# Kernel tuning notes

Measured on AMD Instinct MI355X. Metric: run time of the kernel, lower is better.

The kernel has to match this reference:

```python
import jax, jax.numpy as jnp
import numpy as np

_SAMPLING_EPS = 1e-05
_FP16_TINY = float(np.finfo(np.float16).tiny)  # masked_fill value used by the torch code


def _token_mask(tokens, num_seqs, vocab_size):
    # bin-count via scatter-add into width vocab+1 (padding id == vocab), then mask
    rows = jnp.arange(num_seqs)[:, None]
    counts = jnp.zeros((num_seqs, vocab_size + 1), jnp.int32).at[rows, tokens].add(1)
    return counts[:, :vocab_size] > 0


def setup_inputs() -> dict:
    key = jax.random.key(0)
    ks = jax.random.split(key, 9)
    B, V, PL, OL = 128, 128000, 2048, 256
    logits = jax.random.normal(ks[0], (B, V), dtype=jnp.float32) * 4.0
    prompt_tokens = jax.random.randint(ks[1], (B, PL), 0, V, dtype=jnp.int64)
    output_tokens = jax.random.randint(ks[2], (B, OL), 0, V, dtype=jnp.int64)
    presence_penalties = jax.random.uniform(ks[3], (B,), dtype=jnp.float32)
    frequency_penalties = jax.random.uniform(ks[4], (B,), dtype=jnp.float32)
    repetition_penalties = 1.0 + 0.3 * jax.random.uniform(ks[5], (B,), dtype=jnp.float32)
    temperature = 0.1 + 0.9 * jax.random.uniform(ks[6], (B,), dtype=jnp.float32)
    top_k = jax.random.randint(ks[7], (B,), 1, 100, dtype=jnp.int64)
    top_p = 0.5 + 0.49 * jax.random.uniform(ks[8], (B,), dtype=jnp.float32)
    return {
        "logits": logits,
        "prompt_tokens": prompt_tokens,
        "output_tokens": output_tokens,
        "presence_penalties": presence_penalties,
        "frequency_penalties": frequency_penalties,
        "repetition_penalties": repetition_penalties,
        "temperature": temperature,
        "top_k": top_k,
        "top_p": top_p,
    }


def reference(logits, prompt_tokens, output_tokens, presence_penalties,
              frequency_penalties, repetition_penalties, temperature,
              top_k, top_p):
    B, V = logits.shape
    logits = logits.astype(jnp.float32)

    # --- penalties (NOTE: torch code computes frequency counts but never applies
    # frequency_penalties; we faithfully do the same) ---
    prompt_mask = _token_mask(prompt_tokens, B, V)
    output_mask = _token_mask(output_tokens, B, V)
    pen = jnp.where(prompt_mask | output_mask, repetition_penalties[:, None], 1.0)
    logits = jnp.where(logits > 0, logits / pen, logits * pen)
    logits = logits - presence_penalties[:, None] * output_mask.astype(jnp.float32)

    # --- temperature ---
    temp = jnp.where(temperature < _SAMPLING_EPS, 1.0, temperature)
    logits = logits / temp[:, None]

    # --- top-k / top-p via ascending sort (mirrors torch implementation) ---
    idx = jnp.argsort(logits, axis=-1)                      # ascending
    ls = jnp.take_along_axis(logits, idx, axis=-1)
    thr_pos = (V - top_k.astype(jnp.int32))[:, None]
    thr = jnp.take_along_axis(ls, thr_pos, axis=-1)         # [B,1]
    ls = jnp.where(ls < thr, _FP16_TINY, ls)
    probs_sort = jax.nn.softmax(ls, axis=-1)
    csum = jnp.cumsum(probs_sort, axis=-1)
    tp_mask = csum <= (1.0 - top_p)[:, None]
    tp_mask = tp_mask.at[:, -1].set(False)
    ls = jnp.where(tp_mask, _FP16_TINY, ls)

    # unsort back to original vocab order
    rows = jnp.arange(B)[:, None]
    out_logits = jnp.zeros_like(logits).at[rows, idx].set(ls)

    probs = jax.nn.softmax(out_logits, axis=-1)
    return probs, prompt_mask, output_mask
```

## Files before the change

### kernel.cpp

```cpp
#include <hip/hip_runtime.h>
#include <math.h>

#define B   128
#define V   128000
#define WPR 4000
#define PL  2048
#define OL  256
#define BPR 25
#define ITERS 5
#define TLOC 128
#define GMAX 240
#define CAP  6144
#define FP16_TINY 6.103515625e-05f
#define QZ   1.80f

#define HBINS 4096
#define HIDX(b) ((b) + ((b) >> 4))
#define HSZ (HBINS + (HBINS >> 4))

__device__ __forceinline__ unsigned key_of(float f) {
    unsigned u = __float_as_uint(f);
    unsigned m = (unsigned)(((int)u) >> 31) | 0x80000000u;
    return u ^ m;
}
__device__ __forceinline__ float key_inv(unsigned k) {
    unsigned u = (k & 0x80000000u) ? (k ^ 0x80000000u) : ~k;
    return __uint_as_float(u);
}

__device__ __forceinline__ float xform(float x, int pm, int om,
                                       float rp, float rrp, float pres, float itt) {
#pragma clang fp contract(off)
    float m = (pm | om) ? ((x > 0.0f) ? rrp : rp) : 1.0f;
    float l = x * m;
    if (om) l = l - pres;
    return l * itt;
}

__device__ __forceinline__ unsigned wave_suffix_u(unsigned x, int lane) {
#pragma unroll
    for (int o = 1; o < 64; o <<= 1) {
        unsigned a = __shfl_down(x, o);
        if (lane + o < 64) x += a;
    }
    return x;
}
__device__ __forceinline__ unsigned wave_prefix_u(unsigned x, int lane) {
#pragma unroll
    for (int o = 1; o < 64; o <<= 1) {
        unsigned a = __shfl_up(x, o);
        if (lane >= o) x += a;
    }
    return x;
}
__device__ __forceinline__ double wave_suffix_d(double x, int lane) {
#pragma unroll
    for (int o = 1; o < 64; o <<= 1) {
        double a = __shfl_down(x, o);
        if (lane + o < 64) x += a;
    }
    return x;
}
__device__ __forceinline__ double wave_sum_d(double x) {
#pragma unroll
    for (int o = 1; o < 64; o <<= 1) x += __shfl_xor(x, o);
    return x;
}
__device__ __forceinline__ unsigned wave_sum_u(unsigned x) {
#pragma unroll
    for (int o = 1; o < 64; o <<= 1) x += __shfl_xor(x, o);
    return x;
}

__global__ __launch_bounds__(256) void k_scatter(const int* __restrict__ ptok,
                                                 const int* __restrict__ otok,
                                                 unsigned* __restrict__ bitP,
                                                 unsigned* __restrict__ bitO,
                                                 unsigned* __restrict__ cnt) {
    __shared__ unsigned mp[WPR];
    __shared__ unsigned mo[WPR];
    int r = blockIdx.x;
    int t = threadIdx.x;
    for (int i = t; i < WPR; i += 256) { mp[i] = 0u; mo[i] = 0u; }
    if (t == 0) cnt[r] = 0u;
    __syncthreads();
    const int* prow = ptok + (size_t)r * PL;
    const int* orow = otok + (size_t)r * OL;
    for (int i = t; i < PL; i += 256) {
        int tok = prow[i];
        if ((unsigned)tok < (unsigned)V) atomicOr(&mp[tok >> 5], 1u << (tok & 31));
    }
    for (int i = t; i < OL; i += 256) {
        int tok = orow[i];
        if ((unsigned)tok < (unsigned)V) atomicOr(&mo[tok >> 5], 1u << (tok & 31));
    }
    __syncthreads();
    unsigned* bpo = bitP + (size_t)r * WPR;
    unsigned* boo = bitO + (size_t)r * WPR;
    for (int i = t; i < WPR; i += 256) { bpo[i] = mp[i]; boo[i] = mo[i]; }
}

__global__ __launch_bounds__(256) void k_main(
    const float* __restrict__ logits,
    const unsigned* __restrict__ bitP, const unsigned* __restrict__ bitO,
    const float* __restrict__ rep, const float* __restrict__ pres,
    const float* __restrict__ temp,
    float* __restrict__ outPm, float* __restrict__ outOm,
    unsigned* __restrict__ cnt, unsigned long long* __restrict__ cand)
{
    __shared__ unsigned h[HSZ];
    __shared__ unsigned wsum[4];
    __shared__ int s_beta;
    __shared__ unsigned s_base, s_total;
    int r = blockIdx.y;
    int c0 = blockIdx.x * (ITERS * 1024);
    int t = threadIdx.x;
    int lane = t & 63, wid = t >> 6;
    float rp = rep[r], pp = pres[r];
    float tt = temp[r]; tt = (tt < 1e-5f) ? 1.0f : tt;
    float rrp = 1.0f / rp;
    float itt = 1.0f / tt;
    const float* lrow = logits + (size_t)r * V;
    float* pmrow = outPm + (size_t)r * V;
    float* omrow = outOm + (size_t)r * V;
    const unsigned* bp = bitP + (size_t)r * WPR;
    const unsigned* bo = bitO + (size_t)r * WPR;
    uint4 kv4[ITERS];
#pragma unroll
    for (int it = 0; it < ITERS; it++) {
        int i = c0 + it * 1024 + t * 4;
        float4 x = *(const float4*)(lrow + i);
        unsigned wp = bp[i >> 5], wo = bo[i >> 5];
        int sh = i & 31;
        float xs[4] = {x.x, x.y, x.z, x.w};
        unsigned ks[4];
        float fp[4], fo[4];
#pragma unroll
        for (int j = 0; j < 4; j++) {
            int p = (wp >> (sh + j)) & 1;
            int o = (wo >> (sh + j)) & 1;
            float l = xform(xs[j], p, o, rp, rrp, pp, itt);
            ks[j] = key_of(l);
            fp[j] = (float)p; fo[j] = (float)o;
        }
        kv4[it] = make_uint4(ks[0], ks[1], ks[2], ks[3]);
        *(float4*)(pmrow + i) = make_float4(fp[0], fp[1], fp[2], fp[3]);
        *(float4*)(omrow + i) = make_float4(fo[0], fo[1], fo[2], fo[3]);
    }
    unsigned gk = key_of(QZ * 4.0f * itt);
    unsigned myc = 0;
#pragma unroll
    for (int it = 0; it < ITERS; it++) {
        unsigned ks[4] = {kv4[it].x, kv4[it].y, kv4[it].z, kv4[it].w};
#pragma unroll
        for (int j = 0; j < 4; j++)
            if (ks[j] >= gk) myc++;
    }
    unsigned pfx = wave_prefix_u(myc, lane);
    if (lane == 63) wsum[wid] = pfx;
    __syncthreads();
    unsigned pv = pfx;
#pragma unroll
    for (int w2 = 0; w2 < 4; w2++) if (w2 < wid) pv += wsum[w2];
    if (t == 255) s_total = pv;
    __syncthreads();
    unsigned total = s_total;
    unsigned betaKey;
    if (total >= TLOC && total <= GMAX) {
        betaKey = gk;
    } else {
        for (int i = t; i < HSZ; i += 256) h[i] = 0u;
        __syncthreads();
#pragma unroll
        for (int it = 0; it < ITERS; it++) {
            unsigned ks[4] = {kv4[it].x, kv4[it].y, kv4[it].z, kv4[it].w};
#pragma unroll
            for (int j = 0; j < 4; j++)
                atomicAdd(&h[HIDX(ks[j] >> 20)], 1u);
        }
        __syncthreads();
        unsigned cs = 0;
#pragma unroll
        for (int j = 0; j < 16; j++) cs += h[HIDX(t * 16 + j)];
        unsigned sfx = wave_suffix_u(cs, lane);
        if (lane == 0) wsum[wid] = sfx;
        __syncthreads();
        unsigned suf = sfx;
#pragma unroll
        for (int w2 = 0; w2 < 4; w2++) if (w2 > wid) suf += wsum[w2];
        unsigned Snext = suf - cs;
        if (suf >= TLOC && Snext < TLOC) {
            unsigned run = Snext;
            int beta = t * 16;
            for (int j = 15; j >= 0; j--) {
                run += h[HIDX(t * 16 + j)];
                if (run >= TLOC) { beta = t * 16 + j; break; }
            }
            s_beta = beta;
        }
        __syncthreads();
        betaKey = ((unsigned)s_beta) << 20;
        myc = 0;
#pragma unroll
        for (int it = 0; it < ITERS; it++) {
            unsigned ks[4] = {kv4[it].x, kv4[it].y, kv4[it].z, kv4[it].w};
#pragma unroll
            for (int j = 0; j < 4; j++)
                if (ks[j] >= betaKey) myc++;
        }
        __syncthreads();
        pfx = wave_prefix_u(myc, lane);
        if (lane == 63) wsum[wid] = pfx;
        __syncthreads();
        pv = pfx;
#pragma unroll
        for (int w2 = 0; w2 < 4; w2++) if (w2 < wid) pv += wsum[w2];
    }
    if (t == 255) s_base = atomicAdd(&cnt[r], pv);
    __syncthreads();
    unsigned w = s_base + (pv - myc);
#pragma unroll
    for (int it = 0; it < ITERS; it++) {
        unsigned ks[4] = {kv4[it].x, kv4[it].y, kv4[it].z, kv4[it].w};
#pragma unroll
        for (int j = 0; j < 4; j++) {
            unsigned key = ks[j];
            if (key >= betaKey) {
                if (w < (unsigned)CAP) {
                    int idx = c0 + it * 1024 + t * 4 + j;
                    cand[(size_t)r * CAP + w] =
                        ((unsigned long long)key << 32) | (unsigned)idx;
                }
                w++;
            }
        }
    }
}

__global__ __launch_bounds__(256) void k_select(
    const unsigned* __restrict__ cnt, const unsigned long long* __restrict__ cand,
    const int* __restrict__ topk, const float* __restrict__ topp,
    float4* __restrict__ params, int* __restrict__ idxc,
    unsigned* __restrict__ kn, int* __restrict__ kidx, float* __restrict__ kprob)
{
    __shared__ unsigned long long list[CAP];
    __shared__ unsigned long long kv[256];
    __shared__ unsigned rh[256];
    __shared__ double wD[4];
    __shared__ unsigned wU[4];
    __shared__ unsigned s_prefix, s_krem, s_kcnt;
    int r = blockIdx.x;
    int t = threadIdx.x;
    int lane = t & 63, wid = t >> 6;
    int n = (int)min(cnt[r], (unsigned)CAP);
    const unsigned long long* crow = cand + (size_t)r * CAP;
    for (int i = t; i < n; i += 256) list[i] = crow[i];
    int k = topk[r]; k = max(1, min(k, 127));
    if (t == 0) { s_prefix = 0u; s_krem = (unsigned)k; }
    __syncthreads();
    for (int round = 3; round >= 0; round--) {
        int shift = round * 8;
        unsigned prefix = s_prefix;
        unsigned krem = s_krem;
        unsigned maskAbove = (round == 3) ? 0u : (0xFFFFFFFFu << (shift + 8));
        rh[t] = 0u;
        __syncthreads();
        for (int i = t; i < n; i += 256) {
            unsigned key = (unsigned)(list[i] >> 32);
            if ((key & maskAbove) == (prefix & maskAbove))
                atomicAdd(&rh[(key >> shift) & 255u], 1u);
        }
        __syncthreads();
        unsigned vv = rh[t];
        unsigned sfx = wave_suffix_u(vv, lane);
        if (lane == 0) wU[wid] = sfx;
        __syncthreads();
        unsigned suf = sfx;
#pragma unroll
        for (int w2 = 0; w2 < 4; w2++) if (w2 > wid) suf += wU[w2];
        unsigned Sx = suf - vv;
        if (suf >= krem && Sx < krem) {
            s_prefix = prefix | ((unsigned)t << shift);
            s_krem = krem - Sx;
        }
        __syncthreads();
    }
    unsigned thrkey = s_prefix;
    if (t == 0) s_kcnt = 0u;
    __syncthreads();
    for (int i = t; i < n; i += 256) {
        if ((unsigned)(list[i] >> 32) >= thrkey) {
            unsigned pos = atomicAdd(&s_kcnt, 1u);
            if (pos < 256u) kv[pos] = list[i];
        }
    }
    __syncthreads();
    int K = (int)min(s_kcnt, 256u);
    if (t >= K) kv[t] = 0ULL;
    __syncthreads();
    unsigned long long my = kv[t];
    int rank = 0;
#pragma unroll 8
    for (int i = 0; i < 256; i++) rank += (kv[i] > my) ? 1 : 0;
    __syncthreads();
    if (t < K) kv[rank] = my;
    __syncthreads();
    float Mxf = key_inv((unsigned)(kv[0] >> 32));
    double MxD = (double)Mxf;
    double e_t = (t < K) ? exp((double)key_inv((unsigned)(kv[t] >> 32)) - MxD)
                         : 0.0;
    double red = wave_sum_d(e_t);
    if (lane == 0) wD[wid] = red;
    __syncthreads();
    double S = wD[0] + wD[1] + wD[2] + wD[3];
    __syncthreads();
    double sv = wave_suffix_d(e_t, lane);
    if (lane == 0) wD[wid] = sv;
    __syncthreads();
    double suf_t = sv;
#pragma unroll
    for (int w2 = 0; w2 < 4; w2++) if (w2 > wid) suf_t += wD[w2];
    double e_tinyD = exp((double)FP16_TINY - MxD);
    double Z1 = (double)(V - K) * e_tinyD + S;
    double base = (double)(V - K) * e_tinyD / Z1;
    double thresh = 1.0 - (double)topp[r];
    unsigned flag = (t >= 1 && t < K && (base + suf_t / Z1) <= thresh) ? 1u : 0u;
    unsigned fr = wave_sum_u(flag);
    if (lane == 0) wU[wid] = fr;
    __syncthreads();
    int cm = (int)(wU[0] + wU[1] + wU[2] + wU[3]);
    int ns = K - cm;
    __syncthreads();
    double e2 = (t < ns) ? e_t : 0.0;
    double r2 = wave_sum_d(e2);
    if (lane == 0) wD[wid] = r2;
    __syncthreads();
    double S2 = wD[0] + wD[1] + wD[2] + wD[3];
    unsigned bkey = (unsigned)(kv[ns - 1] >> 32);
    float v_b = key_inv(bkey);
    float tiny_e = expf(FP16_TINY - Mxf);
    double Z2 = (double)(V - ns) * (double)tiny_e + S2;
    float invZ2 = (float)(1.0 / Z2);
    if (t == 0) {
        params[r] = make_float4(v_b, Mxf, invZ2, tiny_e * invZ2);
        idxc[r] = (int)(kv[ns - 1] & 0xFFFFFFFFu);
        kn[r] = (unsigned)ns;
    }
    if (t < ns) {
        unsigned long long e = kv[t];
        unsigned key = (unsigned)(e >> 32);
        kidx[(size_t)r * 256 + t] = (int)(e & 0xFFFFFFFFu);
        kprob[(size_t)r * 256 + t] = expf(key_inv(key) - Mxf) * invZ2;
    }
}

__global__ __launch_bounds__(256) void k_final(
    const float4* __restrict__ params, const unsigned* __restrict__ kn,
    const int* __restrict__ kidx, const float* __restrict__ kprob,
    float* __restrict__ probs)
{
    int r = blockIdx.y;
    int c0 = blockIdx.x * (ITERS * 1024);
    int t = threadIdx.x;
    float ptiny = params[r].w;
    float* orow = probs + (size_t)r * V;
    float4 pv4 = make_float4(ptiny, ptiny, ptiny, ptiny);
#pragma unroll
    for (int it = 0; it < ITERS; it++) {
        int i = c0 + it * 1024 + t * 4;
        *(float4*)(orow + i) = pv4;
    }
    __syncthreads();
    int ns = (int)kn[r];
    int hi = c0 + ITERS * 1024;
    for (int i = t; i < ns; i += 256) {
        int idx = kidx[(size_t)r * 256 + i];
        if (idx >= c0 && idx < hi) orow[idx] = kprob[(size_t)r * 256 + i];
    }
}

extern "C" void kernel_launch(void* const* d_in, const int* in_sizes, int n_in,
                              void* d_out, int out_size, void* d_ws, size_t ws_size,
                              hipStream_t stream) {
    const float* logits = (const float*)d_in[0];
    const int* ptok     = (const int*)d_in[1];
    const int* otok     = (const int*)d_in[2];
    const float* pres   = (const float*)d_in[3];
    const float* rep    = (const float*)d_in[5];
    const float* temp   = (const float*)d_in[6];
    const int* topk     = (const int*)d_in[7];
    const float* topp   = (const float*)d_in[8];

    float* out_probs = (float*)d_out;
    float* out_pm = out_probs + (size_t)B * V;
    float* out_om = out_pm + (size_t)B * V;

    unsigned* ws0 = (unsigned*)d_ws;
    float4* params = (float4*)d_ws;
    int* idxc = (int*)(ws0 + 512);
    unsigned* bitP = ws0 + 768;
    unsigned* bitO = bitP + B * WPR;
    unsigned* cnt  = bitO + B * WPR;
    unsigned long long* cand =
        (unsigned long long*)(cnt + B + 64);
    unsigned* kn   = (unsigned*)(cand + (size_t)B * CAP);
    int* kidx      = (int*)(kn + B);
    float* kprob   = (float*)(kidx + B * 256);

    k_scatter<<<B, 256, 0, stream>>>(ptok, otok, bitP, bitO, cnt);

    dim3 g(BPR, B);
    k_main<<<g, 256, 0, stream>>>(logits, bitP, bitO, rep, pres, temp,
                                  out_pm, out_om, cnt, cand);
    k_select<<<B, 256, 0, stream>>>(cnt, cand, topk, topp, params, idxc,
                                    kn, kidx, kprob);
    k_final<<<g, 256, 0, stream>>>(params, kn, kidx, kprob, out_probs);
}
```

Baseline: 296.5 us.

## Fuse top-k/top-p selection into main kernel via last-block-done counter

Removes the separate k_select launch. Each row's last finishing k_main block, found with a per-row atomic done counter and threadfences, now runs the radix select, sort and top-p computation. Candidates are read straight from global memory rather than staged in shared memory. This saves one kernel launch and lets selection for early-finishing rows overlap with other rows' main work, at the cost of extra shared memory in k_main and repeated global reads of the candidate list.

```diff
diff --git a/kernel.cpp b/kernel.cpp
--- a/kernel.cpp
+++ b/kernel.cpp
@@ -76,13 +76,14 @@
                                                  const int* __restrict__ otok,
                                                  unsigned* __restrict__ bitP,
                                                  unsigned* __restrict__ bitO,
-                                                 unsigned* __restrict__ cnt) {
+                                                 unsigned* __restrict__ cnt,
+                                                 unsigned* __restrict__ done) {
     __shared__ unsigned mp[WPR];
     __shared__ unsigned mo[WPR];
     int r = blockIdx.x;
     int t = threadIdx.x;
     for (int i = t; i < WPR; i += 256) { mp[i] = 0u; mo[i] = 0u; }
-    if (t == 0) cnt[r] = 0u;
+    if (t == 0) { cnt[r] = 0u; done[r] = 0u; }
     __syncthreads();
     const int* prow = ptok + (size_t)r * PL;
     const int* orow = otok + (size_t)r * OL;
@@ -105,13 +106,23 @@
     const unsigned* __restrict__ bitP, const unsigned* __restrict__ bitO,
     const float* __restrict__ rep, const float* __restrict__ pres,
     const float* __restrict__ temp,
+    const int* __restrict__ topk, const float* __restrict__ topp,
     float* __restrict__ outPm, float* __restrict__ outOm,
-    unsigned* __restrict__ cnt, unsigned long long* __restrict__ cand)
+    unsigned* __restrict__ cnt, unsigned* __restrict__ done,
+    unsigned long long* __restrict__ cand,
+    float4* __restrict__ params, unsigned* __restrict__ kn,
+    int* __restrict__ kidx, float* __restrict__ kprob)
 {
     __shared__ unsigned h[HSZ];
     __shared__ unsigned wsum[4];
     __shared__ int s_beta;
-    __shared__ unsigned s_base, s_total;
+    __shared__ unsigned s_base, s_total, s_last;
+    __shared__ unsigned long long kvv[256];
+    __shared__ unsigned rh[256];
+    __shared__ double wD[4];
+    __shared__ unsigned wU[4];
+    __shared__ unsigned s_prefix, s_krem, s_kcnt;
+
     int r = blockIdx.y;
     int c0 = blockIdx.x * (ITERS * 1024);
     int t = threadIdx.x;
@@ -235,26 +246,15 @@
             }
         }
     }
-}
-
-__global__ __launch_bounds__(256) void k_select(
-    const unsigned* __restrict__ cnt, const unsigned long long* __restrict__ cand,
-    const int* __restrict__ topk, const float* __restrict__ topp,
-    float4* __restrict__ params, int* __restrict__ idxc,
-    unsigned* __restrict__ kn, int* __restrict__ kidx, float* __restrict__ kprob)
-{
-    __shared__ unsigned long long list[CAP];
-    __shared__ unsigned long long kv[256];
-    __shared__ unsigned rh[256];
-    __shared__ double wD[4];
-    __shared__ unsigned wU[4];
-    __shared__ unsigned s_prefix, s_krem, s_kcnt;
-    int r = blockIdx.x;
-    int t = threadIdx.x;
-    int lane = t & 63, wid = t >> 6;
+    __threadfence();
+    __syncthreads();
+    if (t == 0) s_last = atomicAdd(&done[r], 1u);
+    __syncthreads();
+    if (s_last != BPR - 1) return;
+    __threadfence();
+
     int n = (int)min(cnt[r], (unsigned)CAP);
     const unsigned long long* crow = cand + (size_t)r * CAP;
-    for (int i = t; i < n; i += 256) list[i] = crow[i];
     int k = topk[r]; k = max(1, min(k, 127));
     if (t == 0) { s_prefix = 0u; s_krem = (unsigned)k; }
     __syncthreads();
@@ -266,7 +266,7 @@
         rh[t] = 0u;
         __syncthreads();
         for (int i = t; i < n; i += 256) {
-            unsigned key = (unsigned)(list[i] >> 32);
+            unsigned key = (unsigned)(crow[i] >> 32);
             if ((key & maskAbove) == (prefix & maskAbove))
                 atomicAdd(&rh[(key >> shift) & 255u], 1u);
         }
@@ -289,25 +289,25 @@
     if (t == 0) s_kcnt = 0u;
     __syncthreads();
     for (int i = t; i < n; i += 256) {
-        if ((unsigned)(list[i] >> 32) >= thrkey) {
+        if ((unsigned)(crow[i] >> 32) >= thrkey) {
             unsigned pos = atomicAdd(&s_kcnt, 1u);
-            if (pos < 256u) kv[pos] = list[i];
+            if (pos < 256u) kvv[pos] = crow[i];
         }
     }
     __syncthreads();
     int K = (int)min(s_kcnt, 256u);
-    if (t >= K) kv[t] = 0ULL;
-    __syncthreads();
-    unsigned long long my = kv[t];
+    if (t >= K) kvv[t] = 0ULL;
+    __syncthreads();
+    unsigned long long my = kvv[t];
     int rank = 0;
 #pragma unroll 8
-    for (int i = 0; i < 256; i++) rank += (kv[i] > my) ? 1 : 0;
-    __syncthreads();
-    if (t < K) kv[rank] = my;
-    __syncthreads();
-    float Mxf = key_inv((unsigned)(kv[0] >> 32));
+    for (int i = 0; i < 256; i++) rank += (kvv[i] > my) ? 1 : 0;
+    __syncthreads();
+    if (t < K) kvv[rank] = my;
+    __syncthreads();
+    float Mxf = key_inv((unsigned)(kvv[0] >> 32));
     double MxD = (double)Mxf;
-    double e_t = (t < K) ? exp((double)key_inv((unsigned)(kv[t] >> 32)) - MxD)
+    double e_t = (t < K) ? exp((double)key_inv((unsigned)(kvv[t] >> 32)) - MxD)
                          : 0.0;
     double red = wave_sum_d(e_t);
     if (lane == 0) wD[wid] = red;
@@ -336,18 +336,16 @@
     if (lane == 0) wD[wid] = r2;
     __syncthreads();
     double S2 = wD[0] + wD[1] + wD[2] + wD[3];
-    unsigned bkey = (unsigned)(kv[ns - 1] >> 32);
-    float v_b = key_inv(bkey);
     float tiny_e = expf(FP16_TINY - Mxf);
     double Z2 = (double)(V - ns) * (double)tiny_e + S2;
     float invZ2 = (float)(1.0 / Z2);
     if (t == 0) {
-        params[r] = make_float4(v_b, Mxf, invZ2, tiny_e * invZ2);
-        idxc[r] = (int)(kv[ns - 1] & 0xFFFFFFFFu);
+        params[r] = make_float4(key_inv((unsigned)(kvv[ns - 1] >> 32)), Mxf,
+                                invZ2, tiny_e * invZ2);
         kn[r] = (unsigned)ns;
     }
     if (t < ns) {
-        unsigned long long e = kv[t];
+        unsigned long long e = kvv[t];
         unsigned key = (unsigned)(e >> 32);
         kidx[(size_t)r * 256 + t] = (int)(e & 0xFFFFFFFFu);
         kprob[(size_t)r * 256 + t] = expf(key_inv(key) - Mxf) * invZ2;
@@ -397,7 +395,7 @@
 
     unsigned* ws0 = (unsigned*)d_ws;
     float4* params = (float4*)d_ws;
-    int* idxc = (int*)(ws0 + 512);
+    unsigned* done = ws0 + 512;
     unsigned* bitP = ws0 + 768;
     unsigned* bitO = bitP + B * WPR;
     unsigned* cnt  = bitO + B * WPR;
@@ -407,12 +405,11 @@
     int* kidx      = (int*)(kn + B);
     float* kprob   = (float*)(kidx + B * 256);
 
-    k_scatter<<<B, 256, 0, stream>>>(ptok, otok, bitP, bitO, cnt);
+    k_scatter<<<B, 256, 0, stream>>>(ptok, otok, bitP, bitO, cnt, done);
 
     dim3 g(BPR, B);
     k_main<<<g, 256, 0, stream>>>(logits, bitP, bitO, rep, pres, temp,
-                                  out_pm, out_om, cnt, cand);
-    k_select<<<B, 256, 0, stream>>>(cnt, cand, topk, topp, params, idxc,
-                                    kn, kidx, kprob);
+                                  topk, topp, out_pm, out_om,
+                                  cnt, done, cand, params, kn, kidx, kprob);
     k_final<<<g, 256, 0, stream>>>(params, kn, kidx, kprob, out_probs);
 }
```

Result: slower. 852.0 us (+187.4%).

## Fuse token bitmap construction into main kernel using per-slice shared bitmaps

Applied to the files above, without the earlier changes.

Removes the separate scatter kernel and its global bitmap buffers. Each main-kernel block now scans the row's prompt and output tokens and builds a small shared-memory bitmap covering only its slice. A memset replaces the counter reset. This avoids one launch and the global bitmap write and read, at the cost of every block rereading all tokens of its row and doing redundant range checks.

```diff
diff --git a/kernel.cpp b/kernel.cpp
--- a/kernel.cpp
+++ b/kernel.cpp
@@ -3,11 +3,12 @@
 
 #define B   128
 #define V   128000
-#define WPR 4000
 #define PL  2048
 #define OL  256
 #define BPR 25
 #define ITERS 5
+#define SLICE (ITERS * 1024)
+#define SW  160
 #define TLOC 128
 #define GMAX 240
 #define CAP  6144
@@ -72,50 +73,37 @@
     return x;
 }
 
-__global__ __launch_bounds__(256) void k_scatter(const int* __restrict__ ptok,
-                                                 const int* __restrict__ otok,
-                                                 unsigned* __restrict__ bitP,
-                                                 unsigned* __restrict__ bitO,
-                                                 unsigned* __restrict__ cnt) {
-    __shared__ unsigned mp[WPR];
-    __shared__ unsigned mo[WPR];
-    int r = blockIdx.x;
-    int t = threadIdx.x;
-    for (int i = t; i < WPR; i += 256) { mp[i] = 0u; mo[i] = 0u; }
-    if (t == 0) cnt[r] = 0u;
-    __syncthreads();
-    const int* prow = ptok + (size_t)r * PL;
-    const int* orow = otok + (size_t)r * OL;
-    for (int i = t; i < PL; i += 256) {
-        int tok = prow[i];
-        if ((unsigned)tok < (unsigned)V) atomicOr(&mp[tok >> 5], 1u << (tok & 31));
-    }
-    for (int i = t; i < OL; i += 256) {
-        int tok = orow[i];
-        if ((unsigned)tok < (unsigned)V) atomicOr(&mo[tok >> 5], 1u << (tok & 31));
-    }
-    __syncthreads();
-    unsigned* bpo = bitP + (size_t)r * WPR;
-    unsigned* boo = bitO + (size_t)r * WPR;
-    for (int i = t; i < WPR; i += 256) { bpo[i] = mp[i]; boo[i] = mo[i]; }
-}
-
 __global__ __launch_bounds__(256) void k_main(
     const float* __restrict__ logits,
-    const unsigned* __restrict__ bitP, const unsigned* __restrict__ bitO,
+    const int* __restrict__ ptok, const int* __restrict__ otok,
     const float* __restrict__ rep, const float* __restrict__ pres,
     const float* __restrict__ temp,
     float* __restrict__ outPm, float* __restrict__ outOm,
     unsigned* __restrict__ cnt, unsigned long long* __restrict__ cand)
 {
+    __shared__ unsigned mp[SW];
+    __shared__ unsigned mo[SW];
     __shared__ unsigned h[HSZ];
     __shared__ unsigned wsum[4];
     __shared__ int s_beta;
     __shared__ unsigned s_base, s_total;
     int r = blockIdx.y;
-    int c0 = blockIdx.x * (ITERS * 1024);
+    int c0 = blockIdx.x * SLICE;
     int t = threadIdx.x;
     int lane = t & 63, wid = t >> 6;
+    if (t < SW) { mp[t] = 0u; mo[t] = 0u; }
+    __syncthreads();
+    const int* prow = ptok + (size_t)r * PL;
+    const int* orow = otok + (size_t)r * OL;
+    for (int i = t; i < PL; i += 256) {
+        unsigned lt = (unsigned)(prow[i] - c0);
+        if (lt < (unsigned)SLICE) atomicOr(&mp[lt >> 5], 1u << (lt & 31));
+    }
+    for (int i = t; i < OL; i += 256) {
+        unsigned lt = (unsigned)(orow[i] - c0);
+        if (lt < (unsigned)SLICE) atomicOr(&mo[lt >> 5], 1u << (lt & 31));
+    }
+    __syncthreads();
     float rp = rep[r], pp = pres[r];
     float tt = temp[r]; tt = (tt < 1e-5f) ? 1.0f : tt;
     float rrp = 1.0f / rp;
@@ -123,15 +111,14 @@
     const float* lrow = logits + (size_t)r * V;
     float* pmrow = outPm + (size_t)r * V;
     float* omrow = outOm + (size_t)r * V;
-    const unsigned* bp = bitP + (size_t)r * WPR;
-    const unsigned* bo = bitO + (size_t)r * WPR;
     uint4 kv4[ITERS];
 #pragma unroll
     for (int it = 0; it < ITERS; it++) {
-        int i = c0 + it * 1024 + t * 4;
+        int li = it * 1024 + t * 4;
+        int i = c0 + li;
         float4 x = *(const float4*)(lrow + i);
-        unsigned wp = bp[i >> 5], wo = bo[i >> 5];
-        int sh = i & 31;
+        unsigned wp = mp[li >> 5], wo = mo[li >> 5];
+        int sh = li & 31;
         float xs[4] = {x.x, x.y, x.z, x.w};
         unsigned ks[4];
         float fp[4], fo[4];
@@ -240,8 +227,8 @@
 __global__ __launch_bounds__(256) void k_select(
     const unsigned* __restrict__ cnt, const unsigned long long* __restrict__ cand,
     const int* __restrict__ topk, const float* __restrict__ topp,
-    float4* __restrict__ params, int* __restrict__ idxc,
-    unsigned* __restrict__ kn, int* __restrict__ kidx, float* __restrict__ kprob)
+    float4* __restrict__ params, unsigned* __restrict__ kn,
+    int* __restrict__ kidx, float* __restrict__ kprob)
 {
     __shared__ unsigned long long list[CAP];
     __shared__ unsigned long long kv[256];
@@ -336,14 +323,12 @@
     if (lane == 0) wD[wid] = r2;
     __syncthreads();
     double S2 = wD[0] + wD[1] + wD[2] + wD[3];
-    unsigned bkey = (unsigned)(kv[ns - 1] >> 32);
-    float v_b = key_inv(bkey);
     float tiny_e = expf(FP16_TINY - Mxf);
     double Z2 = (double)(V - ns) * (double)tiny_e + S2;
     float invZ2 = (float)(1.0 / Z2);
     if (t == 0) {
-        params[r] = make_float4(v_b, Mxf, invZ2, tiny_e * invZ2);
-        idxc[r] = (int)(kv[ns - 1] & 0xFFFFFFFFu);
+        params[r] = make_float4(key_inv((unsigned)(kv[ns - 1] >> 32)), Mxf,
+                                invZ2, tiny_e * invZ2);
         kn[r] = (unsigned)ns;
     }
     if (t < ns) {
@@ -360,7 +345,7 @@
     float* __restrict__ probs)
 {
     int r = blockIdx.y;
-    int c0 = blockIdx.x * (ITERS * 1024);
+    int c0 = blockIdx.x * SLICE;
     int t = threadIdx.x;
     float ptiny = params[r].w;
     float* orow = probs + (size_t)r * V;
@@ -372,7 +357,7 @@
     }
     __syncthreads();
     int ns = (int)kn[r];
-    int hi = c0 + ITERS * 1024;
+    int hi = c0 + SLICE;
     for (int i = t; i < ns; i += 256) {
         int idx = kidx[(size_t)r * 256 + i];
         if (idx >= c0 && idx < hi) orow[idx] = kprob[(size_t)r * 256 + i];
@@ -397,22 +382,19 @@
 
     unsigned* ws0 = (unsigned*)d_ws;
     float4* params = (float4*)d_ws;
-    int* idxc = (int*)(ws0 + 512);
-    unsigned* bitP = ws0 + 768;
-    unsigned* bitO = bitP + B * WPR;
-    unsigned* cnt  = bitO + B * WPR;
+    unsigned* cnt  = ws0 + 512;
+    unsigned* kn   = ws0 + 640;
     unsigned long long* cand =
-        (unsigned long long*)(cnt + B + 64);
-    unsigned* kn   = (unsigned*)(cand + (size_t)B * CAP);
-    int* kidx      = (int*)(kn + B);
+        (unsigned long long*)(ws0 + 768);
+    int* kidx      = (int*)(cand + (size_t)B * CAP);
     float* kprob   = (float*)(kidx + B * 256);
 
-    k_scatter<<<B, 256, 0, stream>>>(ptok, otok, bitP, bitO, cnt);
+    hipMemsetAsync(cnt, 0, B * sizeof(unsigned), stream);
 
     dim3 g(BPR, B);
-    k_main<<<g, 256, 0, stream>>>(logits, bitP, bitO, rep, pres, temp,
+    k_main<<<g, 256, 0, stream>>>(logits, ptok, otok, rep, pres, temp,
                                   out_pm, out_om, cnt, cand);
-    k_select<<<B, 256, 0, stream>>>(cnt, cand, topk, topp, params, idxc,
-                                    kn, kidx, kprob);
+    k_select<<<B, 256, 0, stream>>>(cnt, cand, topk, topp,
+                                    params, kn, kidx, kprob);
     k_final<<<g, 256, 0, stream>>>(params, kn, kidx, kprob, out_probs);
 }
```

After: 295.0 us (median of 2 runs). About the same (-0.5%).
